# Optimization experiments

Hardware: AMD Instinct MI355X
Metric: run time of the kernel (lower is better)

## Reference

```python
import jax, jax.numpy as jnp
import numpy as np

BINS = 256
EPS = 1e-8


def _norm255(x):
    # (x - min) / (max - min) * 255, truncated to int (torch .int())
    mx = jnp.max(x, axis=(2, 3), keepdims=True)
    mn = jnp.min(x, axis=(2, 3), keepdims=True)
    return ((x - mn) / (mx - mn) * 255.0).astype(jnp.int32)


def _hist256(x):
    # x int32 [B,C,H,W] -> per-(b,c) 256-bin histogram [B,C,256] float32
    B, C = x.shape[0], x.shape[1]
    flat = x.reshape(B * C, -1)
    rows = jnp.arange(B * C)[:, None]
    h = jnp.zeros((B * C, BINS), jnp.float32).at[rows, flat].add(1.0)
    return h.reshape(B, C, BINS)


def _entropy(x):
    # faithful to Entropy(): p = hist / (H*W); h = -sum p*log(p+1e-8)
    B, C, H, W = x.shape
    p = _hist256(x) / (H * W)
    h = -jnp.sum(p * jnp.log(p + EPS), axis=2)
    return h[:, :, None, None]  # [B,C,1,1]


def _joint_entropy(x_p, x_ms):
    # Faithful to Joint_entropy's quirky count: for each (i,j) it counts pixels
    # where (x_ms==i AND x_p==j) OR (x_ms!=i AND x_p!=j).
    # count[i,j] = 2*J[i,j] + npix - hist_ms[i] - hist_p[j], J = joint histogram.
    B, C, H, W = x_ms.shape
    npix = H * W
    bins = jnp.arange(BINS)
    M = (x_ms.reshape(B, C, npix)[..., None] == bins).astype(jnp.float32)  # [B,C,P,256]
    P = (x_p.reshape(B, npix)[..., None] == bins).astype(jnp.float32)      # [B,P,256]
    J = jnp.einsum('bcpi,bpj->bcij', M, P)                                  # [B,C,256,256]
    hist_ms = jnp.sum(M, axis=2)  # [B,C,256]
    hist_p = jnp.sum(P, axis=1)   # [B,256]
    count = 2.0 * J + npix - hist_ms[:, :, :, None] - hist_p[:, None, None, :]
    p = count / float(BINS * BINS)  # original divides by 256*256, not npix
    h = -jnp.sum(p * jnp.log(p + EPS), axis=(2, 3))
    return h[:, :, None, None]  # [B,C,1,1]


def _channel(f_p, f_ms):
    B, C, H, W = f_p.shape
    f_p_m = jnp.mean(f_p, axis=1, keepdims=True)  # [B,1,H,W]
    # AdaptiveAvgPool2d((16,16)) with H,W divisible by 16 == block mean
    pooled = f_p.reshape(B, C, 16, H // 16, 16, W // 16).mean(axis=(3, 5))
    f_p_a = jnp.mean(pooled, axis=1, keepdims=True)  # [B,1,16,16]
    f_ms_n = _norm255(f_ms)
    f_p_m_n = _norm255(f_p_m)
    f_p_a_n = _norm255(f_p_a)
    h_ms = _entropy(f_ms_n)                 # [B,C,1,1]
    h_p = _entropy(f_p_m_n)                 # [B,1,1,1]
    h_ms_p = _joint_entropy(f_p_a_n, f_ms_n)  # [B,C,1,1]
    mi = h_p + h_ms - h_ms_p
    mi = jax.nn.softmax(mi, axis=1)  # nn.Softmax() on 4D -> dim=1
    return f_ms + f_ms * mi


def _similarity(f_p, f_ms):
    B, C, H, W = f_p.shape
    f_ms_u = jax.image.resize(f_ms, (B, C, H, W), method='bilinear')
    a = f_ms_u.reshape(B, C, -1)
    b = f_p.reshape(B, C, -1)
    a = a - jnp.mean(a, axis=2, keepdims=True)
    b = b - jnp.mean(b, axis=2, keepdims=True)
    na = jnp.sqrt(jnp.sum(a * a, axis=2))  # [B,C] (ms norms)
    nb = jnp.sqrt(jnp.sum(b * b, axis=2))  # [B,C] (p norms)
    s = jnp.einsum('bcp,bdp->bcd', a, b)   # [B,C,C]
    return s / ((na * nb) / 100.0)[:, :, None]


def _spatial(f_p, f_ms):
    B, C, H, W = f_p.shape
    s_m = _similarity(f_p, f_ms)
    mx = jnp.max(s_m, axis=2)        # [B,C]
    idx = jnp.argmax(s_m, axis=2)    # [B,C] best f_p channel per ms channel
    scores = jax.nn.softmax(mx, axis=1)
    brow = jnp.arange(B)[:, None]
    # group score: sum of softmax scores of ms-channels that picked value v
    g = jnp.zeros((B, C), scores.dtype).at[brow, idx].add(scores)
    cnt = jnp.zeros((B, C), jnp.int32).at[brow, idx].add(1)
    k = jnp.min(jnp.sum(cnt > 0, axis=1))  # min #unique over batch
    min_k = (k + 1) // 2                   # ceil(min_k / 2)
    order = jnp.argsort(-g, axis=1)        # descending group score; absent groups (0) sort last
    sorted_scores = jnp.take_along_axis(g, order, axis=1)  # [B,C]
    pos_mask = jnp.arange(C) < min_k       # keep top min_k positions
    z = jnp.where(pos_mask[None, :], sorted_scores, -jnp.inf)
    w = jax.nn.softmax(z, axis=1)          # softmax over selected scores, 0 elsewhere
    gathered = jnp.take_along_axis(f_p, order[:, :, None, None], axis=1)  # [B,C,H,W]
    mask = jnp.sum(w[:, :, None, None] * jax.nn.sigmoid(gathered), axis=1, keepdims=True)
    return f_p + f_p * mask


def setup_inputs() -> dict:
    key = jax.random.key(0)
    k1, k2 = jax.random.split(key)
    f_p = jax.random.normal(k1, (8, 64, 256, 256), dtype=jnp.float32)
    f_ms = jax.random.normal(k2, (8, 64, 16, 16), dtype=jnp.float32)
    return {"f_p": f_p, "f_ms": f_ms}


def reference(f_p, f_ms):
    rel_ms = _channel(f_p, f_ms)
    rel_p = _spatial(f_p, f_ms)
    return (rel_p, rel_ms)
```

## Files before the change

kernel.cpp:

```cpp
#include <hip/hip_runtime.h>

#define BB 8
#define CC 64
#define HP 256
#define WP 256
#define PP 65536
#define QQ 256

__device__ __forceinline__ unsigned encF(float f) {
    unsigned u = __float_as_uint(f);
    return (u & 0x80000000u) ? ~u : (u | 0x80000000u);
}
__device__ __forceinline__ float decF(unsigned u) {
    unsigned b = (u & 0x80000000u) ? (u ^ 0x80000000u) : ~u;
    return __uint_as_float(b);
}

__device__ __forceinline__ double blockSumD(double v, double* red4) {
    int t = threadIdx.x;
    for (int d = 32; d; d >>= 1) v += __shfl_down(v, d, 64);
    __syncthreads();
    if ((t & 63) == 0) red4[t >> 6] = v;
    __syncthreads();
    double r = red4[0] + red4[1] + red4[2] + red4[3];
    __syncthreads();
    return r;
}

__global__ __launch_bounds__(256) void k0_zero(float* __restrict__ gtent,
                                               double* __restrict__ chsumD,
                                               double* __restrict__ chsumsqD,
                                               int* __restrict__ histpm,
                                               unsigned* __restrict__ minmax) {
    int t = blockIdx.x * 256 + threadIdx.x;
    gtent[t] = 0.f;
    if (t < BB * CC) { chsumD[t] = 0.0; chsumsqD[t] = 0.0; }
    if (t < BB * 256) histpm[t] = 0;
    if (t < BB) { minmax[2 * t] = 0xFFFFFFFFu; minmax[2 * t + 1] = 0u; }
}

__global__ __launch_bounds__(256) void k3_chan(const float* __restrict__ fp,
                                               float* __restrict__ cellsum,
                                               float* __restrict__ gtent,
                                               double* __restrict__ chsumD,
                                               double* __restrict__ chsumsqD) {
    int blk = blockIdx.x;
    int qg = blk & 3, c = (blk >> 2) & 63, b = blk >> 8;
    int x = threadIdx.x, s = x >> 4, r = x & 15;
    const float* src = fp + (size_t)(b * CC + c) * PP;
    __shared__ float tentL[256];
    __shared__ double red4[4];
    tentL[x] = 0.0f;
    __syncthreads();
    float wm, w0, wp;
    if (x <= 7)        { wm = 0.f; w0 = 1.f; wp = 0.f; }
    else if (x >= 248) { wm = 0.f; w0 = 1.f; wp = 0.f; }
    else if (r < 8)    { float fx = ((float)r + 8.5f) * 0.0625f; wm = 1.f - fx; w0 = fx;       wp = 0.f; }
    else               { float fx = ((float)r - 7.5f) * 0.0625f; wm = 0.f;      w0 = 1.f - fx; wp = fx;  }
    double sum = 0.0, ssq = 0.0;
    for (int qi = 0; qi < 4; ++qi) {
        int q = qg * 4 + qi;
        float am = 0.f, a0 = 0.f, ap = 0.f, cs = 0.f;
#pragma unroll
        for (int ry = 0; ry < 16; ++ry) {
            float v = src[(q * 16 + ry) * 256 + x];
            sum += (double)v;
            ssq += (double)v * (double)v;
            cs  += v;
            if ((q == 0 && ry < 8) || (q == 15 && ry >= 8)) {
                a0 += v;
            } else if (ry < 8) {
                float fy = ((float)ry + 8.5f) * 0.0625f;
                am += (1.f - fy) * v; a0 += fy * v;
            } else {
                float fy = ((float)ry - 7.5f) * 0.0625f;
                a0 += (1.f - fy) * v; ap += fy * v;
            }
        }
        float vals[10];
        vals[0] = am * wm; vals[1] = am * w0; vals[2] = am * wp;
        vals[3] = a0 * wm; vals[4] = a0 * w0; vals[5] = a0 * wp;
        vals[6] = ap * wm; vals[7] = ap * w0; vals[8] = ap * wp;
        vals[9] = cs;
#pragma unroll
        for (int d = 8; d; d >>= 1) {
#pragma unroll
            for (int k2 = 0; k2 < 10; ++k2) vals[k2] += __shfl_down(vals[k2], d, 16);
        }
        if (r == 0) {
            if (q > 0) {
                if (s > 0)  atomicAdd(&tentL[(q - 1) * 16 + (s - 1)], vals[0]);
                atomicAdd(&tentL[(q - 1) * 16 + s], vals[1]);
                if (s < 15) atomicAdd(&tentL[(q - 1) * 16 + (s + 1)], vals[2]);
            }
            if (s > 0)  atomicAdd(&tentL[q * 16 + (s - 1)], vals[3]);
            atomicAdd(&tentL[q * 16 + s], vals[4]);
            if (s < 15) atomicAdd(&tentL[q * 16 + (s + 1)], vals[5]);
            if (q < 15) {
                if (s > 0)  atomicAdd(&tentL[(q + 1) * 16 + (s - 1)], vals[6]);
                atomicAdd(&tentL[(q + 1) * 16 + s], vals[7]);
                if (s < 15) atomicAdd(&tentL[(q + 1) * 16 + (s + 1)], vals[8]);
            }
            cellsum[(size_t)(b * CC + c) * QQ + q * 16 + s] = vals[9];
        }
    }
    __syncthreads();
    int row = x >> 4;
    int rlo = qg * 4 - 1; if (rlo < 0) rlo = 0;
    int rhi = qg * 4 + 4; if (rhi > 15) rhi = 15;
    if (row >= rlo && row <= rhi) {
        atomicAdd(&gtent[(size_t)(b * CC + c) * QQ + x], tentL[x]);
    }
    double st = blockSumD(sum, red4);
    double sq = blockSumD(ssq, red4);
    if (x == 0) {
        atomicAdd(&chsumD[b * CC + c], st);
        atomicAdd(&chsumsqD[b * CC + c], sq);
    }
}

__global__ __launch_bounds__(256) void k4_ms(const float* __restrict__ fms,
                                             int* __restrict__ msn,
                                             int* __restrict__ histms,
                                             float* __restrict__ hmsE,
                                             float* __restrict__ naArr,
                                             float* __restrict__ mssum) {
    int blk = blockIdx.x, b = blk >> 6, c = blk & 63, t = threadIdx.x;
    __shared__ float m[256];
    __shared__ int hist[256];
    __shared__ double red4[4];
    __shared__ double U[256];
    __shared__ unsigned umn, umx;
    float v = fms[(size_t)(b * CC + c) * QQ + t];
    m[t] = v;
    hist[t] = 0;
    if (t == 0) { umn = 0xFFFFFFFFu; umx = 0u; }
    float mn = v, mx = v;
    for (int d = 32; d; d >>= 1) {
        mn = fminf(mn, __shfl_down(mn, d, 64));
        mx = fmaxf(mx, __shfl_down(mx, d, 64));
    }
    __syncthreads();
    if ((t & 63) == 0) { atomicMin(&umn, encF(mn)); atomicMax(&umx, encF(mx)); }
    __syncthreads();
    mn = decF(umn); mx = decF(umx);
    int bin = (int)((v - mn) / (mx - mn) * 255.0f);
    bin = min(max(bin, 0), 255);
    msn[(size_t)(b * CC + c) * QQ + t] = bin;
    atomicAdd(&hist[bin], 1);
    __syncthreads();
    histms[(size_t)(b * CC + c) * QQ + t] = hist[t];
    float pf = (float)hist[t] * (1.0f / 256.0f);
    double term = -(double)(pf * __logf(pf + 1e-8f));
    double h = blockSumD(term, red4);
    if (t == 0) hmsE[b * CC + c] = (float)h;
    int i = t >> 4, j = t & 15;
    double kdj = (j == 0 || j == 15) ? 13.328125 : 10.65625;
    double mv = (double)m[t];
    double uu = kdj * mv + 2.671875 * ((j > 0 ? (double)m[t - 1] : 0.0) +
                                       (j < 15 ? (double)m[t + 1] : 0.0));
    U[t] = uu;
    __syncthreads();
    double kdi = (i == 0 || i == 15) ? 13.328125 : 10.65625;
    double vv = kdi * U[t] + 2.671875 * ((i > 0 ? U[t - 16] : 0.0) +
                                         (i < 15 ? U[t + 16] : 0.0));
    double sq = blockSumD(mv * vv, red4);
    double msm = blockSumD(mv, red4);
    if (t == 0) {
        mssum[b * CC + c] = (float)msm;
        double meanu = msm * (1.0 / 256.0);
        double na2 = sq - 65536.0 * meanu * meanu;
        naArr[b * CC + c] = (float)sqrt(na2 > 0.0 ? na2 : 0.0);
    }
}

__global__ __launch_bounds__(256) void k8_smax(const float* __restrict__ fms,
                                               const float* __restrict__ gtent,
                                               const float* __restrict__ mssum,
                                               const double* __restrict__ chsumD,
                                               const double* __restrict__ chsumsqD,
                                               const float* __restrict__ naArr,
                                               float* __restrict__ mxArr,
                                               int* __restrict__ idxArr) {
    int blk = blockIdx.x, b = blk >> 6, c = blk & 63, t = threadIdx.x;
    __shared__ float msrow[256];
    __shared__ double part[256];
    __shared__ double sval[64];
    msrow[t] = fms[(size_t)(b * CC + c) * QQ + t];
    __syncthreads();
    int d = t >> 2, pr = t & 3;
    const float* g = gtent + (size_t)(b * CC + d) * QQ + pr * 64;
    const float* mr = msrow + pr * 64;
    double acc = 0.0;
    for (int q2 = 0; q2 < 64; ++q2) acc += (double)mr[q2] * (double)g[q2];
    part[t] = acc;
    __syncthreads();
    if (t < 64) {
        double meanu = (double)mssum[b * CC + c] * (1.0 / 256.0);
        double meanp = chsumD[b * CC + t] * (1.0 / 65536.0);
        sval[t] = part[t * 4] + part[t * 4 + 1] + part[t * 4 + 2] + part[t * 4 + 3]
                  - 65536.0 * meanu * meanp;
    }
    __syncthreads();
    if (t == 0) {
        double best = sval[0]; int bi2 = 0;
        for (int dd = 1; dd < 64; ++dd) { if (sval[dd] > best) { best = sval[dd]; bi2 = dd; } }
        double nac = (double)naArr[b * CC + c];
        double sc_ = chsumD[b * CC + c];
        double sq_ = chsumsqD[b * CC + c];
        double nb2 = sq_ - sc_ * sc_ * (1.0 / 65536.0);
        double nbc = sqrt(nb2 > 0.0 ? nb2 : 0.0);
        mxArr[b * CC + c] = (float)(best * 100.0 / (nac * nbc));
        idxArr[b * CC + c] = bi2;
    }
}

__global__ __launch_bounds__(512) void k9_small(const float* __restrict__ mxArr,
                                                const int* __restrict__ idxArr,
                                                float* __restrict__ wsel,
                                                int* __restrict__ chanA,
                                                int* __restrict__ minkA) {
    __shared__ double sc[8][64];
    __shared__ double gs[8][64];
    __shared__ int idxS[8][64];
    __shared__ int ordv[8][64];
    __shared__ int uarr[8];
    __shared__ int mkS;
    int t = threadIdx.x;
    int b = t >> 6, c = t & 63;
    double v = (double)mxArr[b * 64 + c];
    double mx = v;
    for (int d = 32; d; d >>= 1) mx = fmax(mx, __shfl_down(mx, d, 64));
    mx = __shfl(mx, 0, 64);
    double e = exp(v - mx);
    double s = e;
    for (int d = 32; d; d >>= 1) s += __shfl_down(s, d, 64);
    s = __shfl(s, 0, 64);
    sc[b][c] = e / s;
    idxS[b][c] = idxArr[b * 64 + c];
    __syncthreads();
    double g = 0.0; int cnt = 0;
    for (int c2 = 0; c2 < 64; ++c2) {
        if (idxS[b][c2] == c) { g += sc[b][c2]; cnt++; }
    }
    gs[b][c] = g;
    unsigned long long ball = __ballot(cnt > 0);
    if (c == 0) uarr[b] = __popcll(ball);
    __syncthreads();
    if (t == 0) {
        int k = uarr[0];
        for (int b2 = 1; b2 < 8; ++b2) k = min(k, uarr[b2]);
        mkS = (k + 1) >> 1;
        minkA[0] = mkS;
    }
    __syncthreads();
    int rk = 0;
    double myg = gs[b][c];
    for (int c3 = 0; c3 < 64; ++c3) {
        double a = gs[b][c3];
        if (a > myg || (a == myg && c3 < c)) rk++;
    }
    ordv[b][rk] = c;
    __syncthreads();
    int mk = mkS;
    double z0 = gs[b][ordv[b][0]];
    double ee = (c < mk) ? exp(gs[b][ordv[b][c]] - z0) : 0.0;
    double se = ee;
    for (int d = 32; d; d >>= 1) se += __shfl_down(se, d, 64);
    se = __shfl(se, 0, 64);
    if (c < mk) {
        wsel[b * 64 + c] = (float)(ee / se);
        chanA[b * 64 + c] = ordv[b][c];
    }
}

__global__ __launch_bounds__(256) void kM_mask(const float* __restrict__ fp,
                                               const float* __restrict__ wsel,
                                               const int* __restrict__ chanA,
                                               const int* __restrict__ minkA,
                                               float* __restrict__ maskB) {
    int b = blockIdx.y;
    int i4 = blockIdx.x * 256 + threadIdx.x;
    int mk = minkA[0];
    const float4* src = (const float4*)(fp + (size_t)b * CC * PP);
    float mx0 = 0.f, mx1 = 0.f, mx2 = 0.f, mx3 = 0.f;
    for (int i = 0; i < mk; ++i) {
        int ch = chanA[b * 64 + i];
        float wv = wsel[b * 64 + i];
        float4 v = src[(size_t)ch * (PP / 4) + i4];
        mx0 += wv * (1.0f / (1.0f + __expf(-v.x)));
        mx1 += wv * (1.0f / (1.0f + __expf(-v.y)));
        mx2 += wv * (1.0f / (1.0f + __expf(-v.z)));
        mx3 += wv * (1.0f / (1.0f + __expf(-v.w)));
    }
    ((float4*)(maskB + (size_t)b * PP))[i4] = make_float4(mx0, mx1, mx2, mx3);
}

__global__ __launch_bounds__(256) void k10_relp(const float* __restrict__ fp,
                                                const float* __restrict__ maskB,
                                                float* __restrict__ outp,
                                                float* __restrict__ fpm,
                                                unsigned* __restrict__ minmax) {
    int b = blockIdx.y;
    int i4 = blockIdx.x * 256 + threadIdx.x;
    const float4* src = (const float4*)(fp + (size_t)b * CC * PP);
    float4 mk4 = ((const float4*)(maskB + (size_t)b * PP))[i4];
    float sx = 0.f, sy = 0.f, sz = 0.f, sw = 0.f;
    float4* dst = (float4*)(outp + (size_t)b * CC * PP);
    for (int c2 = 0; c2 < CC; ++c2) {
        float4 v = src[(size_t)c2 * (PP / 4) + i4];
        sx += v.x; sy += v.y; sz += v.z; sw += v.w;
        float4 o;
        o.x = v.x + v.x * mk4.x;
        o.y = v.y + v.y * mk4.y;
        o.z = v.z + v.z * mk4.z;
        o.w = v.w + v.w * mk4.w;
        dst[(size_t)c2 * (PP / 4) + i4] = o;
    }
    const float inv = 1.0f / 64.0f;
    float4 m; m.x = sx * inv; m.y = sy * inv; m.z = sz * inv; m.w = sw * inv;
    ((float4*)(fpm + (size_t)b * PP))[i4] = m;
    float mn = fminf(fminf(m.x, m.y), fminf(m.z, m.w));
    float mxv = fmaxf(fmaxf(m.x, m.y), fmaxf(m.z, m.w));
    for (int d = 32; d; d >>= 1) {
        mn = fminf(mn, __shfl_down(mn, d, 64));
        mxv = fmaxf(mxv, __shfl_down(mxv, d, 64));
    }
    __shared__ unsigned smn, smx;
    if (threadIdx.x == 0) { smn = 0xFFFFFFFFu; smx = 0u; }
    __syncthreads();
    if ((threadIdx.x & 63) == 0) { atomicMin(&smn, encF(mn)); atomicMax(&smx, encF(mxv)); }
    __syncthreads();
    if (threadIdx.x == 0) { atomicMin(&minmax[2 * b], smn); atomicMax(&minmax[2 * b + 1], smx); }
}

__global__ __launch_bounds__(256) void k2a_hist(const float* __restrict__ fpm,
                                                const unsigned* __restrict__ minmax,
                                                int* __restrict__ histpm) {
    int b = blockIdx.y;
    __shared__ int h[256];
    h[threadIdx.x] = 0;
    __syncthreads();
    float mn = decF(minmax[2 * b]);
    float mx = decF(minmax[2 * b + 1]);
    float dd = mx - mn;
    int i4 = blockIdx.x * 256 + threadIdx.x;
    float4 v = ((const float4*)(fpm + (size_t)b * PP))[i4];
    int b0 = (int)((v.x - mn) / dd * 255.0f);
    int b1 = (int)((v.y - mn) / dd * 255.0f);
    int b2 = (int)((v.z - mn) / dd * 255.0f);
    int b3 = (int)((v.w - mn) / dd * 255.0f);
    b0 = min(max(b0, 0), 255); b1 = min(max(b1, 0), 255);
    b2 = min(max(b2, 0), 255); b3 = min(max(b3, 0), 255);
    atomicAdd(&h[b0], 1); atomicAdd(&h[b1], 1);
    atomicAdd(&h[b2], 1); atomicAdd(&h[b3], 1);
    __syncthreads();
    atomicAdd(&histpm[b * 256 + threadIdx.x], h[threadIdx.x]);
}

__global__ __launch_bounds__(256) void kCb_small(const int* __restrict__ histpm,
                                                 const float* __restrict__ cellsum,
                                                 float* __restrict__ hpE,
                                                 int* __restrict__ pan,
                                                 int* __restrict__ histp) {
    int b = blockIdx.x, t = threadIdx.x;
    __shared__ int hist[256];
    __shared__ double red4[4];
    __shared__ unsigned umn, umx;
    hist[t] = 0;
    if (t == 0) { umn = 0xFFFFFFFFu; umx = 0u; }
    int n = histpm[b * 256 + t];
    float p = (float)n * (1.0f / 65536.0f);
    double term = -(double)(p * __logf(p + 1e-8f));
    double h = blockSumD(term, red4);
    if (t == 0) hpE[b] = (float)h;
    double acc = 0.0;
    for (int c = 0; c < CC; ++c) acc += (double)cellsum[(size_t)(b * CC + c) * QQ + t];
    float pa = (float)(acc * (1.0 / 256.0) * (1.0 / 64.0));
    float mn2 = pa, mx2 = pa;
    for (int d = 32; d; d >>= 1) {
        mn2 = fminf(mn2, __shfl_down(mn2, d, 64));
        mx2 = fmaxf(mx2, __shfl_down(mx2, d, 64));
    }
    __syncthreads();
    if ((t & 63) == 0) { atomicMin(&umn, encF(mn2)); atomicMax(&umx, encF(mx2)); }
    __syncthreads();
    mn2 = decF(umn); mx2 = decF(umx);
    int bin = (int)((pa - mn2) / (mx2 - mn2) * 255.0f);
    bin = min(max(bin, 0), 255);
    pan[b * QQ + t] = bin;
    atomicAdd(&hist[bin], 1);
    __syncthreads();
    histp[b * 256 + t] = hist[t];
}

__global__ __launch_bounds__(256) void k6_joint(const int* __restrict__ msn,
                                                const int* __restrict__ pan,
                                                const int* __restrict__ histms,
                                                const int* __restrict__ histp,
                                                float* __restrict__ hjoint) {
    int blk = blockIdx.x, b = blk >> 6, c = blk & 63, t = threadIdx.x;
    __shared__ int key[256], hms[256], hp[256];
    __shared__ double red4[4];
    int iv = msn[(size_t)(b * CC + c) * QQ + t];
    int jv = pan[b * QQ + t];
    key[t] = (iv << 8) | jv;
    hms[t] = histms[(size_t)(b * CC + c) * QQ + t];
    hp[t] = histp[b * 256 + t];
    __syncthreads();
    unsigned long long w0_ = 0, w1_ = 0, w2_ = 0, w3_ = 0;
    for (int p = 0; p < 256; ++p) {
        int k2 = key[p];
        if ((k2 >> 8) == t) {
            int j = k2 & 255;
            unsigned long long bit = 1ull << (j & 63);
            int w = j >> 6;
            if (w == 0) w0_ |= bit; else if (w == 1) w1_ |= bit;
            else if (w == 2) w2_ |= bit; else w3_ |= bit;
        }
    }
    double acc = 0.0;
    int basei = 256 - hms[t];
    unsigned long long words[4] = { w0_, w1_, w2_, w3_ };
#pragma unroll
    for (int w = 0; w < 4; ++w) {
        unsigned long long word = words[w];
        for (int jj = 0; jj < 64; ++jj) {
            if (!((word >> jj) & 1ull)) {
                int cnt = basei - hp[w * 64 + jj];
                float pf = (float)cnt * (1.0f / 65536.0f);
                acc -= (double)(pf * __logf(pf + 1e-8f));
            }
        }
    }
    int myk = key[t], n = 0; bool first = true;
    for (int p = 0; p < 256; ++p) {
        int k2 = key[p];
        if (k2 == myk) { n++; if (p < t) first = false; }
    }
    if (first) {
        int cnt = 2 * n + 256 - hms[myk >> 8] - hp[myk & 255];
        float pf = (float)cnt * (1.0f / 65536.0f);
        acc -= (double)(pf * __logf(pf + 1e-8f));
    }
    double h = blockSumD(acc, red4);
    if (t == 0) hjoint[b * CC + c] = (float)h;
}

__global__ __launch_bounds__(256) void k7_relms(const float* __restrict__ fms,
                                                const float* __restrict__ hmsE,
                                                const float* __restrict__ hpE,
                                                const float* __restrict__ hjoint,
                                                float* __restrict__ out2) {
    int b = blockIdx.x, t = threadIdx.x;
    __shared__ double mi[64];
    if (t < 64) mi[t] = (double)hpE[b] + (double)hmsE[b * CC + t] - (double)hjoint[b * CC + t];
    __syncthreads();
    if (t == 0) {
        double mxv = mi[0];
        for (int c2 = 1; c2 < 64; ++c2) if (mi[c2] > mxv) mxv = mi[c2];
        double s = 0.0;
        for (int c2 = 0; c2 < 64; ++c2) { mi[c2] = exp(mi[c2] - mxv); s += mi[c2]; }
        for (int c2 = 0; c2 < 64; ++c2) mi[c2] /= s;
    }
    __syncthreads();
    const float* src = fms + (size_t)b * CC * QQ;
    float* dst = out2 + (size_t)b * CC * QQ;
    for (int e = t; e < CC * QQ; e += 256) {
        float v = src[e];
        float miv = (float)mi[e >> 8];
        dst[e] = v + v * miv;
    }
}

extern "C" void kernel_launch(void* const* d_in, const int* in_sizes, int n_in,
                              void* d_out, int out_size, void* d_ws, size_t ws_size,
                              hipStream_t stream) {
    const float* fp = (const float*)d_in[0];
    const float* fms = (const float*)d_in[1];
    float* out = (float*)d_out;

    char* p = (char*)d_ws;
    auto alloc = [&](size_t bytes) { void* r = (void*)p; p += (bytes + 255) & ~(size_t)255; return r; };

    float* fpm      = (float*)alloc((size_t)BB * PP * 4);
    float* maskB    = (float*)alloc((size_t)BB * PP * 4);
    float* cellsum  = (float*)alloc((size_t)BB * CC * QQ * 4);
    float* gtent    = (float*)alloc((size_t)BB * CC * QQ * 4);
    double* chsumD  = (double*)alloc((size_t)BB * CC * 8);
    double* chsumsqD= (double*)alloc((size_t)BB * CC * 8);
    unsigned* minmax= (unsigned*)alloc((size_t)BB * 2 * 4);
    int* histpm     = (int*)alloc((size_t)BB * 256 * 4);
    int* msn        = (int*)alloc((size_t)BB * CC * QQ * 4);
    int* histms     = (int*)alloc((size_t)BB * CC * 256 * 4);
    int* histp      = (int*)alloc((size_t)BB * 256 * 4);
    int* pan        = (int*)alloc((size_t)BB * QQ * 4);
    float* hmsE     = (float*)alloc((size_t)BB * CC * 4);
    float* hpE      = (float*)alloc((size_t)BB * 4);
    float* hjoint   = (float*)alloc((size_t)BB * CC * 4);
    float* naArr    = (float*)alloc((size_t)BB * CC * 4);
    float* mssum    = (float*)alloc((size_t)BB * CC * 4);
    float* mxArr    = (float*)alloc((size_t)BB * CC * 4);
    int* idxArr     = (int*)alloc((size_t)BB * CC * 4);
    float* wsel     = (float*)alloc((size_t)BB * CC * 4);
    int* chanA      = (int*)alloc((size_t)BB * CC * 4);
    int* minkA      = (int*)alloc(256);

    float* out_relp  = out;
    float* out_relms = out + (size_t)BB * CC * PP;

    k0_zero<<<512, 256, 0, stream>>>(gtent, chsumD, chsumsqD, histpm, minmax);
    k3_chan<<<2048, 256, 0, stream>>>(fp, cellsum, gtent, chsumD, chsumsqD);
    k4_ms<<<512, 256, 0, stream>>>(fms, msn, histms, hmsE, naArr, mssum);
    k8_smax<<<512, 256, 0, stream>>>(fms, gtent, mssum, chsumD, chsumsqD, naArr, mxArr, idxArr);
    k9_small<<<1, 512, 0, stream>>>(mxArr, idxArr, wsel, chanA, minkA);
    kM_mask<<<dim3(64, 8), 256, 0, stream>>>(fp, wsel, chanA, minkA, maskB);
    k10_relp<<<dim3(64, 8), 256, 0, stream>>>(fp, maskB, out_relp, fpm, minmax);
    k2a_hist<<<dim3(64, 8), 256, 0, stream>>>(fpm, minmax, histpm);
    kCb_small<<<8, 256, 0, stream>>>(histpm, cellsum, hpE, pan, histp);
    k6_joint<<<512, 256, 0, stream>>>(msn, pan, histms, histp, hjoint);
    k7_relms<<<8, 256, 0, stream>>>(fms, hmsE, hpE, hjoint, out_relms);
}
```

Baseline: 413.8 us.

## Fuse small kernels and reorder schedule to cut launch count

```diff
diff --git a/kernel.cpp b/kernel.cpp
--- a/kernel.cpp
+++ b/kernel.cpp
@@ -27,191 +27,263 @@
     return r;
 }
 
-__global__ __launch_bounds__(256) void k0_zero(float* __restrict__ gtent,
-                                               double* __restrict__ chsumD,
-                                               double* __restrict__ chsumsqD,
-                                               int* __restrict__ histpm,
-                                               unsigned* __restrict__ minmax) {
-    int t = blockIdx.x * 256 + threadIdx.x;
-    gtent[t] = 0.f;
-    if (t < BB * CC) { chsumD[t] = 0.0; chsumsqD[t] = 0.0; }
-    if (t < BB * 256) histpm[t] = 0;
-    if (t < BB) { minmax[2 * t] = 0xFFFFFFFFu; minmax[2 * t + 1] = 0u; }
-}
-
-__global__ __launch_bounds__(256) void k3_chan(const float* __restrict__ fp,
-                                               float* __restrict__ cellsum,
-                                               float* __restrict__ gtent,
-                                               double* __restrict__ chsumD,
-                                               double* __restrict__ chsumsqD) {
+__global__ __launch_bounds__(256) void k34_fused(const float* __restrict__ fp,
+                                                 const float* __restrict__ fms,
+                                                 float* __restrict__ cellsum,
+                                                 float* __restrict__ gtent,
+                                                 double* __restrict__ chsumD,
+                                                 double* __restrict__ chsumsqD,
+                                                 int* __restrict__ msn,
+                                                 int* __restrict__ histms,
+                                                 float* __restrict__ hmsE,
+                                                 float* __restrict__ naArr,
+                                                 float* __restrict__ mssum) {
     int blk = blockIdx.x;
-    int qg = blk & 3, c = (blk >> 2) & 63, b = blk >> 8;
-    int x = threadIdx.x, s = x >> 4, r = x & 15;
-    const float* src = fp + (size_t)(b * CC + c) * PP;
-    __shared__ float tentL[256];
-    __shared__ double red4[4];
-    tentL[x] = 0.0f;
-    __syncthreads();
-    float wm, w0, wp;
-    if (x <= 7)        { wm = 0.f; w0 = 1.f; wp = 0.f; }
-    else if (x >= 248) { wm = 0.f; w0 = 1.f; wp = 0.f; }
-    else if (r < 8)    { float fx = ((float)r + 8.5f) * 0.0625f; wm = 1.f - fx; w0 = fx;       wp = 0.f; }
-    else               { float fx = ((float)r - 7.5f) * 0.0625f; wm = 0.f;      w0 = 1.f - fx; wp = fx;  }
-    double sum = 0.0, ssq = 0.0;
-    for (int qi = 0; qi < 4; ++qi) {
-        int q = qg * 4 + qi;
-        float am = 0.f, a0 = 0.f, ap = 0.f, cs = 0.f;
+    if (blk < 2048) {
+        int qg = blk & 3, c = (blk >> 2) & 63, b = blk >> 8;
+        int x = threadIdx.x, s = x >> 4, r = x & 15;
+        const float* src = fp + (size_t)(b * CC + c) * PP;
+        __shared__ float tentL[256];
+        __shared__ double red4[4];
+        tentL[x] = 0.0f;
+        __syncthreads();
+        float wm, w0, wp;
+        if (x <= 7)        { wm = 0.f; w0 = 1.f; wp = 0.f; }
+        else if (x >= 248) { wm = 0.f; w0 = 1.f; wp = 0.f; }
+        else if (r < 8)    { float fx = ((float)r + 8.5f) * 0.0625f; wm = 1.f - fx; w0 = fx;       wp = 0.f; }
+        else               { float fx = ((float)r - 7.5f) * 0.0625f; wm = 0.f;      w0 = 1.f - fx; wp = fx;  }
+        double sum = 0.0, ssq = 0.0;
+        for (int qi = 0; qi < 4; ++qi) {
+            int q = qg * 4 + qi;
+            float am = 0.f, a0 = 0.f, ap = 0.f, cs = 0.f;
 #pragma unroll
-        for (int ry = 0; ry < 16; ++ry) {
-            float v = src[(q * 16 + ry) * 256 + x];
-            sum += (double)v;
-            ssq += (double)v * (double)v;
-            cs  += v;
-            if ((q == 0 && ry < 8) || (q == 15 && ry >= 8)) {
-                a0 += v;
-            } else if (ry < 8) {
-                float fy = ((float)ry + 8.5f) * 0.0625f;
-                am += (1.f - fy) * v; a0 += fy * v;
-            } else {
-                float fy = ((float)ry - 7.5f) * 0.0625f;
-                a0 += (1.f - fy) * v; ap += fy * v;
+            for (int ry = 0; ry < 16; ++ry) {
+                float v = src[(q * 16 + ry) * 256 + x];
+                sum += (double)v;
+                ssq += (double)v * (double)v;
+                cs  += v;
+                if ((q == 0 && ry < 8) || (q == 15 && ry >= 8)) {
+                    a0 += v;
+                } else if (ry < 8) {
+                    float fy = ((float)ry + 8.5f) * 0.0625f;
+                    am += (1.f - fy) * v; a0 += fy * v;
+                } else {
+                    float fy = ((float)ry - 7.5f) * 0.0625f;
+                    a0 += (1.f - fy) * v; ap += fy * v;
+                }
             }
-        }
-        float vals[10];
-        vals[0] = am * wm; vals[1] = am * w0; vals[2] = am * wp;
-        vals[3] = a0 * wm; vals[4] = a0 * w0; vals[5] = a0 * wp;
-        vals[6] = ap * wm; vals[7] = ap * w0; vals[8] = ap * wp;
-        vals[9] = cs;
+            float vals[10];
+            vals[0] = am * wm; vals[1] = am * w0; vals[2] = am * wp;
+            vals[3] = a0 * wm; vals[4] = a0 * w0; vals[5] = a0 * wp;
+            vals[6] = ap * wm; vals[7] = ap * w0; vals[8] = ap * wp;
+            vals[9] = cs;
 #pragma unroll
-        for (int d = 8; d; d >>= 1) {
+            for (int d = 8; d; d >>= 1) {
 #pragma unroll
-            for (int k2 = 0; k2 < 10; ++k2) vals[k2] += __shfl_down(vals[k2], d, 16);
-        }
-        if (r == 0) {
-            if (q > 0) {
-                if (s > 0)  atomicAdd(&tentL[(q - 1) * 16 + (s - 1)], vals[0]);
-                atomicAdd(&tentL[(q - 1) * 16 + s], vals[1]);
-                if (s < 15) atomicAdd(&tentL[(q - 1) * 16 + (s + 1)], vals[2]);
+                for (int k2 = 0; k2 < 10; ++k2) vals[k2] += __shfl_down(vals[k2], d, 16);
             }
-            if (s > 0)  atomicAdd(&tentL[q * 16 + (s - 1)], vals[3]);
-            atomicAdd(&tentL[q * 16 + s], vals[4]);
-            if (s < 15) atomicAdd(&tentL[q * 16 + (s + 1)], vals[5]);
-            if (q < 15) {
-                if (s > 0)  atomicAdd(&tentL[(q + 1) * 16 + (s - 1)], vals[6]);
-                atomicAdd(&tentL[(q + 1) * 16 + s], vals[7]);
-                if (s < 15) atomicAdd(&tentL[(q + 1) * 16 + (s + 1)], vals[8]);
+            if (r == 0) {
+                if (q > 0) {
+                    if (s > 0)  atomicAdd(&tentL[(q - 1) * 16 + (s - 1)], vals[0]);
+                    atomicAdd(&tentL[(q - 1) * 16 + s], vals[1]);
+                    if (s < 15) atomicAdd(&tentL[(q - 1) * 16 + (s + 1)], vals[2]);
+                }
+                if (s > 0)  atomicAdd(&tentL[q * 16 + (s - 1)], vals[3]);
+                atomicAdd(&tentL[q * 16 + s], vals[4]);
+                if (s < 15) atomicAdd(&tentL[q * 16 + (s + 1)], vals[5]);
+                if (q < 15) {
+                    if (s > 0)  atomicAdd(&tentL[(q + 1) * 16 + (s - 1)], vals[6]);
+                    atomicAdd(&tentL[(q + 1) * 16 + s], vals[7]);
+                    if (s < 15) atomicAdd(&tentL[(q + 1) * 16 + (s + 1)], vals[8]);
+                }
+                cellsum[(size_t)(b * CC + c) * QQ + q * 16 + s] = vals[9];
             }
-            cellsum[(size_t)(b * CC + c) * QQ + q * 16 + s] = vals[9];
-        }
-    }
-    __syncthreads();
-    int row = x >> 4;
-    int rlo = qg * 4 - 1; if (rlo < 0) rlo = 0;
-    int rhi = qg * 4 + 4; if (rhi > 15) rhi = 15;
-    if (row >= rlo && row <= rhi) {
-        atomicAdd(&gtent[(size_t)(b * CC + c) * QQ + x], tentL[x]);
-    }
-    double st = blockSumD(sum, red4);
-    double sq = blockSumD(ssq, red4);
-    if (x == 0) {
-        atomicAdd(&chsumD[b * CC + c], st);
-        atomicAdd(&chsumsqD[b * CC + c], sq);
-    }
-}
-
-__global__ __launch_bounds__(256) void k4_ms(const float* __restrict__ fms,
-                                             int* __restrict__ msn,
-                                             int* __restrict__ histms,
-                                             float* __restrict__ hmsE,
-                                             float* __restrict__ naArr,
-                                             float* __restrict__ mssum) {
-    int blk = blockIdx.x, b = blk >> 6, c = blk & 63, t = threadIdx.x;
-    __shared__ float m[256];
+        }
+        __syncthreads();
+        int row = x >> 4;
+        int rlo = qg * 4 - 1; if (rlo < 0) rlo = 0;
+        int rhi = qg * 4 + 4; if (rhi > 15) rhi = 15;
+        if (row >= rlo && row <= rhi) {
+            atomicAdd(&gtent[(size_t)(b * CC + c) * QQ + x], tentL[x]);
+        }
+        double st = blockSumD(sum, red4);
+        double sq = blockSumD(ssq, red4);
+        if (x == 0) {
+            atomicAdd(&chsumD[b * CC + c], st);
+            atomicAdd(&chsumsqD[b * CC + c], sq);
+        }
+    } else {
+        int blk2 = blk - 2048, b = blk2 >> 6, c = blk2 & 63, t = threadIdx.x;
+        __shared__ float m[256];
+        __shared__ int hist[256];
+        __shared__ double red4[4];
+        __shared__ double U[256];
+        __shared__ unsigned umn, umx;
+        float v = fms[(size_t)(b * CC + c) * QQ + t];
+        m[t] = v;
+        hist[t] = 0;
+        if (t == 0) { umn = 0xFFFFFFFFu; umx = 0u; }
+        float mn = v, mx = v;
+        for (int d = 32; d; d >>= 1) {
+            mn = fminf(mn, __shfl_down(mn, d, 64));
+            mx = fmaxf(mx, __shfl_down(mx, d, 64));
+        }
+        __syncthreads();
+        if ((t & 63) == 0) { atomicMin(&umn, encF(mn)); atomicMax(&umx, encF(mx)); }
+        __syncthreads();
+        mn = decF(umn); mx = decF(umx);
+        int bin = (int)((v - mn) / (mx - mn) * 255.0f);
+        bin = min(max(bin, 0), 255);
+        msn[(size_t)(b * CC + c) * QQ + t] = bin;
+        atomicAdd(&hist[bin], 1);
+        __syncthreads();
+        histms[(size_t)(b * CC + c) * QQ + t] = hist[t];
+        float pf = (float)hist[t] * (1.0f / 256.0f);
+        double term = -(double)(pf * __logf(pf + 1e-8f));
+        double h = blockSumD(term, red4);
+        if (t == 0) hmsE[b * CC + c] = (float)h;
+        int i = t >> 4, j = t & 15;
+        double kdj = (j == 0 || j == 15) ? 13.328125 : 10.65625;
+        double mv = (double)m[t];
+        double uu = kdj * mv + 2.671875 * ((j > 0 ? (double)m[t - 1] : 0.0) +
+                                           (j < 15 ? (double)m[t + 1] : 0.0));
+        U[t] = uu;
+        __syncthreads();
+        double kdi = (i == 0 || i == 15) ? 13.328125 : 10.65625;
+        double vv = kdi * U[t] + 2.671875 * ((i > 0 ? U[t - 16] : 0.0) +
+                                             (i < 15 ? U[t + 16] : 0.0));
+        double sq = blockSumD(mv * vv, red4);
+        double msm = blockSumD(mv, red4);
+        if (t == 0) {
+            mssum[b * CC + c] = (float)msm;
+            double meanu = msm * (1.0 / 256.0);
+            double na2 = sq - 65536.0 * meanu * meanu;
+            naArr[b * CC + c] = (float)sqrt(na2 > 0.0 ? na2 : 0.0);
+        }
+    }
+}
+
+__global__ __launch_bounds__(256) void kC5_pa(const float* __restrict__ cellsum,
+                                              int* __restrict__ pan,
+                                              int* __restrict__ histp) {
+    int b = blockIdx.x, t = threadIdx.x;
     __shared__ int hist[256];
-    __shared__ double red4[4];
-    __shared__ double U[256];
     __shared__ unsigned umn, umx;
-    float v = fms[(size_t)(b * CC + c) * QQ + t];
-    m[t] = v;
     hist[t] = 0;
     if (t == 0) { umn = 0xFFFFFFFFu; umx = 0u; }
-    float mn = v, mx = v;
+    double acc = 0.0;
+    for (int c = 0; c < CC; ++c) acc += (double)cellsum[(size_t)(b * CC + c) * QQ + t];
+    float pa = (float)(acc * (1.0 / 256.0) * (1.0 / 64.0));
+    float mn2 = pa, mx2 = pa;
     for (int d = 32; d; d >>= 1) {
-        mn = fminf(mn, __shfl_down(mn, d, 64));
-        mx = fmaxf(mx, __shfl_down(mx, d, 64));
-    }
-    __syncthreads();
-    if ((t & 63) == 0) { atomicMin(&umn, encF(mn)); atomicMax(&umx, encF(mx)); }
-    __syncthreads();
-    mn = decF(umn); mx = decF(umx);
-    int bin = (int)((v - mn) / (mx - mn) * 255.0f);
+        mn2 = fminf(mn2, __shfl_down(mn2, d, 64));
+        mx2 = fmaxf(mx2, __shfl_down(mx2, d, 64));
+    }
+    __syncthreads();
+    if ((t & 63) == 0) { atomicMin(&umn, encF(mn2)); atomicMax(&umx, encF(mx2)); }
+    __syncthreads();
+    mn2 = decF(umn); mx2 = decF(umx);
+    int bin = (int)((pa - mn2) / (mx2 - mn2) * 255.0f);
     bin = min(max(bin, 0), 255);
-    msn[(size_t)(b * CC + c) * QQ + t] = bin;
+    pan[b * QQ + t] = bin;
     atomicAdd(&hist[bin], 1);
     __syncthreads();
-    histms[(size_t)(b * CC + c) * QQ + t] = hist[t];
-    float pf = (float)hist[t] * (1.0f / 256.0f);
-    double term = -(double)(pf * __logf(pf + 1e-8f));
-    double h = blockSumD(term, red4);
-    if (t == 0) hmsE[b * CC + c] = (float)h;
-    int i = t >> 4, j = t & 15;
-    double kdj = (j == 0 || j == 15) ? 13.328125 : 10.65625;
-    double mv = (double)m[t];
-    double uu = kdj * mv + 2.671875 * ((j > 0 ? (double)m[t - 1] : 0.0) +
-                                       (j < 15 ? (double)m[t + 1] : 0.0));
-    U[t] = uu;
-    __syncthreads();
-    double kdi = (i == 0 || i == 15) ? 13.328125 : 10.65625;
-    double vv = kdi * U[t] + 2.671875 * ((i > 0 ? U[t - 16] : 0.0) +
-                                         (i < 15 ? U[t + 16] : 0.0));
-    double sq = blockSumD(mv * vv, red4);
-    double msm = blockSumD(mv, red4);
-    if (t == 0) {
-        mssum[b * CC + c] = (float)msm;
-        double meanu = msm * (1.0 / 256.0);
-        double na2 = sq - 65536.0 * meanu * meanu;
-        naArr[b * CC + c] = (float)sqrt(na2 > 0.0 ? na2 : 0.0);
-    }
-}
-
-__global__ __launch_bounds__(256) void k8_smax(const float* __restrict__ fms,
-                                               const float* __restrict__ gtent,
-                                               const float* __restrict__ mssum,
-                                               const double* __restrict__ chsumD,
-                                               const double* __restrict__ chsumsqD,
-                                               const float* __restrict__ naArr,
-                                               float* __restrict__ mxArr,
-                                               int* __restrict__ idxArr) {
-    int blk = blockIdx.x, b = blk >> 6, c = blk & 63, t = threadIdx.x;
-    __shared__ float msrow[256];
-    __shared__ double part[256];
-    __shared__ double sval[64];
-    msrow[t] = fms[(size_t)(b * CC + c) * QQ + t];
-    __syncthreads();
-    int d = t >> 2, pr = t & 3;
-    const float* g = gtent + (size_t)(b * CC + d) * QQ + pr * 64;
-    const float* mr = msrow + pr * 64;
-    double acc = 0.0;
-    for (int q2 = 0; q2 < 64; ++q2) acc += (double)mr[q2] * (double)g[q2];
-    part[t] = acc;
-    __syncthreads();
-    if (t < 64) {
-        double meanu = (double)mssum[b * CC + c] * (1.0 / 256.0);
-        double meanp = chsumD[b * CC + t] * (1.0 / 65536.0);
-        sval[t] = part[t * 4] + part[t * 4 + 1] + part[t * 4 + 2] + part[t * 4 + 3]
-                  - 65536.0 * meanu * meanp;
-    }
-    __syncthreads();
-    if (t == 0) {
-        double best = sval[0]; int bi2 = 0;
-        for (int dd = 1; dd < 64; ++dd) { if (sval[dd] > best) { best = sval[dd]; bi2 = dd; } }
-        double nac = (double)naArr[b * CC + c];
-        double sc_ = chsumD[b * CC + c];
-        double sq_ = chsumsqD[b * CC + c];
-        double nb2 = sq_ - sc_ * sc_ * (1.0 / 65536.0);
-        double nbc = sqrt(nb2 > 0.0 ? nb2 : 0.0);
-        mxArr[b * CC + c] = (float)(best * 100.0 / (nac * nbc));
-        idxArr[b * CC + c] = bi2;
+    histp[b * 256 + t] = hist[t];
+}
+
+__global__ __launch_bounds__(256) void k86_fused(const float* __restrict__ fms,
+                                                 const float* __restrict__ gtent,
+                                                 const float* __restrict__ mssum,
+                                                 const double* __restrict__ chsumD,
+                                                 const double* __restrict__ chsumsqD,
+                                                 const float* __restrict__ naArr,
+                                                 const int* __restrict__ msn,
+                                                 const int* __restrict__ pan,
+                                                 const int* __restrict__ histms,
+                                                 const int* __restrict__ histp,
+                                                 float* __restrict__ mxArr,
+                                                 int* __restrict__ idxArr,
+                                                 float* __restrict__ hjoint) {
+    int blk0 = blockIdx.x;
+    if (blk0 < 512) {
+        int blk = blk0, b = blk >> 6, c = blk & 63, t = threadIdx.x;
+        __shared__ float msrow[256];
+        __shared__ double part[256];
+        __shared__ double sval[64];
+        msrow[t] = fms[(size_t)(b * CC + c) * QQ + t];
+        __syncthreads();
+        int d = t >> 2, pr = t & 3;
+        const float* g = gtent + (size_t)(b * CC + d) * QQ + pr * 64;
+        const float* mr = msrow + pr * 64;
+        double acc = 0.0;
+        for (int q2 = 0; q2 < 64; ++q2) acc += (double)mr[q2] * (double)g[q2];
+        part[t] = acc;
+        __syncthreads();
+        if (t < 64) {
+            double meanu = (double)mssum[b * CC + c] * (1.0 / 256.0);
+            double meanp = chsumD[b * CC + t] * (1.0 / 65536.0);
+            sval[t] = part[t * 4] + part[t * 4 + 1] + part[t * 4 + 2] + part[t * 4 + 3]
+                      - 65536.0 * meanu * meanp;
+        }
+        __syncthreads();
+        if (t == 0) {
+            double best = sval[0]; int bi2 = 0;
+            for (int dd = 1; dd < 64; ++dd) { if (sval[dd] > best) { best = sval[dd]; bi2 = dd; } }
+            double nac = (double)naArr[b * CC + c];
+            double sc_ = chsumD[b * CC + c];
+            double sq_ = chsumsqD[b * CC + c];
+            double nb2 = sq_ - sc_ * sc_ * (1.0 / 65536.0);
+            double nbc = sqrt(nb2 > 0.0 ? nb2 : 0.0);
+            mxArr[b * CC + c] = (float)(best * 100.0 / (nac * nbc));
+            idxArr[b * CC + c] = bi2;
+        }
+    } else {
+        int blk = blk0 - 512, b = blk >> 6, c = blk & 63, t = threadIdx.x;
+        __shared__ int key[256], hms[256], hp[256];
+        __shared__ double red4[4];
+        int iv = msn[(size_t)(b * CC + c) * QQ + t];
+        int jv = pan[b * QQ + t];
+        key[t] = (iv << 8) | jv;
+        hms[t] = histms[(size_t)(b * CC + c) * QQ + t];
+        hp[t] = histp[b * 256 + t];
+        __syncthreads();
+        unsigned long long w0_ = 0, w1_ = 0, w2_ = 0, w3_ = 0;
+        for (int p = 0; p < 256; ++p) {
+            int k2 = key[p];
+            if ((k2 >> 8) == t) {
+                int j = k2 & 255;
+                unsigned long long bit = 1ull << (j & 63);
+                int w = j >> 6;
+                if (w == 0) w0_ |= bit; else if (w == 1) w1_ |= bit;
+                else if (w == 2) w2_ |= bit; else w3_ |= bit;
+            }
+        }
+        double acc = 0.0;
+        int basei = 256 - hms[t];
+        unsigned long long words[4] = { w0_, w1_, w2_, w3_ };
+#pragma unroll
+        for (int w = 0; w < 4; ++w) {
+            unsigned long long word = words[w];
+            for (int jj = 0; jj < 64; ++jj) {
+                if (!((word >> jj) & 1ull)) {
+                    int cnt = basei - hp[w * 64 + jj];
+                    float pf = (float)cnt * (1.0f / 65536.0f);
+                    acc -= (double)(pf * __logf(pf + 1e-8f));
+                }
+            }
+        }
+        int myk = key[t], n = 0; bool first = true;
+        for (int p = 0; p < 256; ++p) {
+            int k2 = key[p];
+            if (k2 == myk) { n++; if (p < t) first = false; }
+        }
+        if (first) {
+            int cnt = 2 * n + 256 - hms[myk >> 8] - hp[myk & 255];
+            float pf = (float)cnt * (1.0f / 65536.0f);
+            acc -= (double)(pf * __logf(pf + 1e-8f));
+        }
+        double h = blockSumD(acc, red4);
+        if (t == 0) hjoint[b * CC + c] = (float)h;
     }
 }
 
@@ -327,134 +399,49 @@
         mxv = fmaxf(mxv, __shfl_down(mxv, d, 64));
     }
     __shared__ unsigned smn, smx;
-    if (threadIdx.x == 0) { smn = 0xFFFFFFFFu; smx = 0u; }
-    __syncthreads();
-    if ((threadIdx.x & 63) == 0) { atomicMin(&smn, encF(mn)); atomicMax(&smx, encF(mxv)); }
-    __syncthreads();
-    if (threadIdx.x == 0) { atomicMin(&minmax[2 * b], smn); atomicMax(&minmax[2 * b + 1], smx); }
-}
-
-__global__ __launch_bounds__(256) void k2a_hist(const float* __restrict__ fpm,
+    if (threadIdx.x == 0) { smn = 0u; smx = 0u; }
+    __syncthreads();
+    if ((threadIdx.x & 63) == 0) { atomicMax(&smn, ~encF(mn)); atomicMax(&smx, encF(mxv)); }
+    __syncthreads();
+    if (threadIdx.x == 0) { atomicMax(&minmax[2 * b], smn); atomicMax(&minmax[2 * b + 1], smx); }
+}
+
+__global__ __launch_bounds__(256) void kF_relms(const float* __restrict__ fpm,
                                                 const unsigned* __restrict__ minmax,
-                                                int* __restrict__ histpm) {
-    int b = blockIdx.y;
-    __shared__ int h[256];
-    h[threadIdx.x] = 0;
-    __syncthreads();
-    float mn = decF(minmax[2 * b]);
-    float mx = decF(minmax[2 * b + 1]);
-    float dd = mx - mn;
-    int i4 = blockIdx.x * 256 + threadIdx.x;
-    float4 v = ((const float4*)(fpm + (size_t)b * PP))[i4];
-    int b0 = (int)((v.x - mn) / dd * 255.0f);
-    int b1 = (int)((v.y - mn) / dd * 255.0f);
-    int b2 = (int)((v.z - mn) / dd * 255.0f);
-    int b3 = (int)((v.w - mn) / dd * 255.0f);
-    b0 = min(max(b0, 0), 255); b1 = min(max(b1, 0), 255);
-    b2 = min(max(b2, 0), 255); b3 = min(max(b3, 0), 255);
-    atomicAdd(&h[b0], 1); atomicAdd(&h[b1], 1);
-    atomicAdd(&h[b2], 1); atomicAdd(&h[b3], 1);
-    __syncthreads();
-    atomicAdd(&histpm[b * 256 + threadIdx.x], h[threadIdx.x]);
-}
-
-__global__ __launch_bounds__(256) void kCb_small(const int* __restrict__ histpm,
-                                                 const float* __restrict__ cellsum,
-                                                 float* __restrict__ hpE,
-                                                 int* __restrict__ pan,
-                                                 int* __restrict__ histp) {
+                                                const float* __restrict__ fms,
+                                                const float* __restrict__ hmsE,
+                                                const float* __restrict__ hjoint,
+                                                float* __restrict__ out2) {
     int b = blockIdx.x, t = threadIdx.x;
     __shared__ int hist[256];
     __shared__ double red4[4];
-    __shared__ unsigned umn, umx;
+    __shared__ double mi[64];
+    __shared__ float hpEs;
     hist[t] = 0;
-    if (t == 0) { umn = 0xFFFFFFFFu; umx = 0u; }
-    int n = histpm[b * 256 + t];
+    __syncthreads();
+    float mn = decF(~minmax[2 * b]);
+    float mx = decF(minmax[2 * b + 1]);
+    float dd = mx - mn;
+    const float4* src = (const float4*)(fpm + (size_t)b * PP);
+    for (int k = 0; k < 64; ++k) {
+        float4 v = src[t + k * 256];
+        int b0 = (int)((v.x - mn) / dd * 255.0f);
+        int b1 = (int)((v.y - mn) / dd * 255.0f);
+        int b2 = (int)((v.z - mn) / dd * 255.0f);
+        int b3 = (int)((v.w - mn) / dd * 255.0f);
+        b0 = min(max(b0, 0), 255); b1 = min(max(b1, 0), 255);
+        b2 = min(max(b2, 0), 255); b3 = min(max(b3, 0), 255);
+        atomicAdd(&hist[b0], 1); atomicAdd(&hist[b1], 1);
+        atomicAdd(&hist[b2], 1); atomicAdd(&hist[b3], 1);
+    }
+    __syncthreads();
+    int n = hist[t];
     float p = (float)n * (1.0f / 65536.0f);
     double term = -(double)(p * __logf(p + 1e-8f));
     double h = blockSumD(term, red4);
-    if (t == 0) hpE[b] = (float)h;
-    double acc = 0.0;
-    for (int c = 0; c < CC; ++c) acc += (double)cellsum[(size_t)(b * CC + c) * QQ + t];
-    float pa = (float)(acc * (1.0 / 256.0) * (1.0 / 64.0));
-    float mn2 = pa, mx2 = pa;
-    for (int d = 32; d; d >>= 1) {
-        mn2 = fminf(mn2, __shfl_down(mn2, d, 64));
-        mx2 = fmaxf(mx2, __shfl_down(mx2, d, 64));
-    }
-    __syncthreads();
-    if ((t & 63) == 0) { atomicMin(&umn, encF(mn2)); atomicMax(&umx, encF(mx2)); }
-    __syncthreads();
-    mn2 = decF(umn); mx2 = decF(umx);
-    int bin = (int)((pa - mn2) / (mx2 - mn2) * 255.0f);
-    bin = min(max(bin, 0), 255);
-    pan[b * QQ + t] = bin;
-    atomicAdd(&hist[bin], 1);
-    __syncthreads();
-    histp[b * 256 + t] = hist[t];
-}
-
-__global__ __launch_bounds__(256) void k6_joint(const int* __restrict__ msn,
-                                                const int* __restrict__ pan,
-                                                const int* __restrict__ histms,
-                                                const int* __restrict__ histp,
-                                                float* __restrict__ hjoint) {
-    int blk = blockIdx.x, b = blk >> 6, c = blk & 63, t = threadIdx.x;
-    __shared__ int key[256], hms[256], hp[256];
-    __shared__ double red4[4];
-    int iv = msn[(size_t)(b * CC + c) * QQ + t];
-    int jv = pan[b * QQ + t];
-    key[t] = (iv << 8) | jv;
-    hms[t] = histms[(size_t)(b * CC + c) * QQ + t];
-    hp[t] = histp[b * 256 + t];
-    __syncthreads();
-    unsigned long long w0_ = 0, w1_ = 0, w2_ = 0, w3_ = 0;
-    for (int p = 0; p < 256; ++p) {
-        int k2 = key[p];
-        if ((k2 >> 8) == t) {
-            int j = k2 & 255;
-            unsigned long long bit = 1ull << (j & 63);
-            int w = j >> 6;
-            if (w == 0) w0_ |= bit; else if (w == 1) w1_ |= bit;
-            else if (w == 2) w2_ |= bit; else w3_ |= bit;
-        }
-    }
-    double acc = 0.0;
-    int basei = 256 - hms[t];
-    unsigned long long words[4] = { w0_, w1_, w2_, w3_ };
-#pragma unroll
-    for (int w = 0; w < 4; ++w) {
-        unsigned long long word = words[w];
-        for (int jj = 0; jj < 64; ++jj) {
-            if (!((word >> jj) & 1ull)) {
-                int cnt = basei - hp[w * 64 + jj];
-                float pf = (float)cnt * (1.0f / 65536.0f);
-                acc -= (double)(pf * __logf(pf + 1e-8f));
-            }
-        }
-    }
-    int myk = key[t], n = 0; bool first = true;
-    for (int p = 0; p < 256; ++p) {
-        int k2 = key[p];
-        if (k2 == myk) { n++; if (p < t) first = false; }
-    }
-    if (first) {
-        int cnt = 2 * n + 256 - hms[myk >> 8] - hp[myk & 255];
-        float pf = (float)cnt * (1.0f / 65536.0f);
-        acc -= (double)(pf * __logf(pf + 1e-8f));
-    }
-    double h = blockSumD(acc, red4);
-    if (t == 0) hjoint[b * CC + c] = (float)h;
-}
-
-__global__ __launch_bounds__(256) void k7_relms(const float* __restrict__ fms,
-                                                const float* __restrict__ hmsE,
-                                                const float* __restrict__ hpE,
-                                                const float* __restrict__ hjoint,
-                                                float* __restrict__ out2) {
-    int b = blockIdx.x, t = threadIdx.x;
-    __shared__ double mi[64];
-    if (t < 64) mi[t] = (double)hpE[b] + (double)hmsE[b * CC + t] - (double)hjoint[b * CC + t];
+    if (t == 0) hpEs = (float)h;
+    __syncthreads();
+    if (t < 64) mi[t] = (double)hpEs + (double)hmsE[b * CC + t] - (double)hjoint[b * CC + t];
     __syncthreads();
     if (t == 0) {
         double mxv = mi[0];
@@ -464,12 +451,12 @@
         for (int c2 = 0; c2 < 64; ++c2) mi[c2] /= s;
     }
     __syncthreads();
-    const float* src = fms + (size_t)b * CC * QQ;
-    float* dst = out2 + (size_t)b * CC * QQ;
+    const float* srcm = fms + (size_t)b * CC * QQ;
+    float* dstm = out2 + (size_t)b * CC * QQ;
     for (int e = t; e < CC * QQ; e += 256) {
-        float v = src[e];
+        float v = srcm[e];
         float miv = (float)mi[e >> 8];
-        dst[e] = v + v * miv;
+        dstm[e] = v + v * miv;
     }
 }
 
@@ -486,17 +473,17 @@
     float* fpm      = (float*)alloc((size_t)BB * PP * 4);
     float* maskB    = (float*)alloc((size_t)BB * PP * 4);
     float* cellsum  = (float*)alloc((size_t)BB * CC * QQ * 4);
+    char* zbeg = p;
     float* gtent    = (float*)alloc((size_t)BB * CC * QQ * 4);
     double* chsumD  = (double*)alloc((size_t)BB * CC * 8);
     double* chsumsqD= (double*)alloc((size_t)BB * CC * 8);
     unsigned* minmax= (unsigned*)alloc((size_t)BB * 2 * 4);
-    int* histpm     = (int*)alloc((size_t)BB * 256 * 4);
+    size_t zlen = (size_t)(p - zbeg);
     int* msn        = (int*)alloc((size_t)BB * CC * QQ * 4);
     int* histms     = (int*)alloc((size_t)BB * CC * 256 * 4);
     int* histp      = (int*)alloc((size_t)BB * 256 * 4);
     int* pan        = (int*)alloc((size_t)BB * QQ * 4);
     float* hmsE     = (float*)alloc((size_t)BB * CC * 4);
-    float* hpE      = (float*)alloc((size_t)BB * 4);
     float* hjoint   = (float*)alloc((size_t)BB * CC * 4);
     float* naArr    = (float*)alloc((size_t)BB * CC * 4);
     float* mssum    = (float*)alloc((size_t)BB * CC * 4);
@@ -509,15 +496,14 @@
     float* out_relp  = out;
     float* out_relms = out + (size_t)BB * CC * PP;
 
-    k0_zero<<<512, 256, 0, stream>>>(gtent, chsumD, chsumsqD, histpm, minmax);
-    k3_chan<<<2048, 256, 0, stream>>>(fp, cellsum, gtent, chsumD, chsumsqD);
-    k4_ms<<<512, 256, 0, stream>>>(fms, msn, histms, hmsE, naArr, mssum);
-    k8_smax<<<512, 256, 0, stream>>>(fms, gtent, mssum, chsumD, chsumsqD, naArr, mxArr, idxArr);
+    hipMemsetAsync(zbeg, 0, zlen, stream);
+    k34_fused<<<2560, 256, 0, stream>>>(fp, fms, cellsum, gtent, chsumD, chsumsqD,
+                                        msn, histms, hmsE, naArr, mssum);
+    kC5_pa<<<8, 256, 0, stream>>>(cellsum, pan, histp);
+    k86_fused<<<1024, 256, 0, stream>>>(fms, gtent, mssum, chsumD, chsumsqD, naArr,
+                                        msn, pan, histms, histp, mxArr, idxArr, hjoint);
     k9_small<<<1, 512, 0, stream>>>(mxArr, idxArr, wsel, chanA, minkA);
     kM_mask<<<dim3(64, 8), 256, 0, stream>>>(fp, wsel, chanA, minkA, maskB);
     k10_relp<<<dim3(64, 8), 256, 0, stream>>>(fp, maskB, out_relp, fpm, minmax);
-    k2a_hist<<<dim3(64, 8), 256, 0, stream>>>(fpm, minmax, histpm);
-    kCb_small<<<8, 256, 0, stream>>>(histpm, cellsum, hpE, pan, histp);
-    k6_joint<<<512, 256, 0, stream>>>(msn, pan, histms, histp, hjoint);
-    k7_relms<<<8, 256, 0, stream>>>(fms, hmsE, hpE, hjoint, out_relms);
-}
+    kF_relms<<<8, 256, 0, stream>>>(fpm, minmax, fms, hmsE, hjoint, out_relms);
+}
```

Measured after the change: 423.8 us. 1.02x slower.
